# Optimization experiments

Measured on AMD Instinct MI355X. Metric: run time of the kernel, lower is better.

## Reference

```python
import jax, jax.numpy as jnp
import numpy as np

H = 256       # lstm_hidden_size
B = 64        # batch
L = 128       # sequence length
LABEL = 128   # slot label size


def setup_inputs() -> dict:
    key = jax.random.key(0)
    ks = jax.random.split(key, 8)
    s = 1.0 / np.sqrt(H)  # torch LSTM/Linear uniform init scale
    return {
        "x": jax.random.normal(ks[0], (B, L, 2 * H), jnp.float32),
        "hi": jax.random.normal(ks[1], (B, L, 2 * H), jnp.float32),
        "W_ih": jax.random.uniform(ks[2], (4 * H, 5 * H), jnp.float32, -s, s),
        "W_hh": jax.random.uniform(ks[3], (4 * H, H), jnp.float32, -s, s),
        "b_ih": jax.random.uniform(ks[4], (4 * H,), jnp.float32, -s, s),
        "b_hh": jax.random.uniform(ks[5], (4 * H,), jnp.float32, -s, s),
        "W_fc": jax.random.uniform(ks[6], (LABEL, H), jnp.float32, -s, s),
        "b_fc": jax.random.uniform(ks[7], (LABEL,), jnp.float32, -s, s),
    }


def reference(x, hi, W_ih, W_hh, b_ih, b_hh, W_fc, b_fc):
    # dropout_rate = 0.0 -> dropout is identity.
    h_dim = W_hh.shape[1]
    bias = b_ih + b_hh  # (4H,)

    # x cat hi: (B, L, 4H) -> time-major (L, B, 4H)
    feats = jnp.transpose(jnp.concatenate([x, hi], axis=-1), (1, 0, 2))

    def cell(hc, inp):
        # PyTorch feeds (batch,1,5H) into a seq-major LSTM, so each batch
        # element is one recurrent step with batch-size 1.
        h, c = hc  # (H,), (H,)
        g = inp @ W_ih.T + h @ W_hh.T + bias  # (4H,)
        i, f, gg, o = jnp.split(g, 4)
        i = jax.nn.sigmoid(i)
        f = jax.nn.sigmoid(f)
        gg = jnp.tanh(gg)
        o = jax.nn.sigmoid(o)
        c_new = f * c + i * gg
        h_new = o * jnp.tanh(c_new)
        return (h_new, c_new), h_new

    def step(carry, x_t):
        # x_t: (B, 4H); out_prev: (B, H) = previous timestep's LSTM outputs
        h, c, out_prev = carry
        inp = jnp.concatenate([x_t, out_prev], axis=-1)  # (B, 5H)
        (h, c), outs = jax.lax.scan(cell, (h, c), inp)   # scan over batch dim
        return (h, c, outs), outs

    h0 = jnp.zeros((h_dim,), x.dtype)
    c0 = jnp.zeros((h_dim,), x.dtype)
    out0 = jnp.zeros((x.shape[0], h_dim), x.dtype)  # dec_init_out

    (_, _, _), all_out = jax.lax.scan(step, (h0, c0, out0), feats)  # (L, B, H)
    output = jnp.transpose(all_out, (1, 0, 2))  # (B, L, H)
    return output @ W_fc.T + b_fc  # (B, L, LABEL)
```

## Files before the change

### kernel.cpp

```cpp
#include <hip/hip_runtime.h>
#include <math.h>

#define H    256
#define BB   64
#define LL   128
#define LBL  128
#define NSTEP (BB*LL)
#define GDIM (4*H)
#define KDIM (4*H)
#define W5   (5*H)
#define NWG  16
#define NROW (NSTEP + 64)

typedef unsigned long long ull;

#define SW(j) ((j) + ((j) >> 4))

__global__ void k_init(ull* __restrict__ HT)
{
    const int r = blockIdx.x;
    const int e = threadIdx.x;
    HT[(ull)r * H + e] = ((ull)(unsigned)r << 32);
}

__global__ __launch_bounds__(256) void k_pre(const float* __restrict__ x,
                                             const float* __restrict__ hi,
                                             const float* __restrict__ Wih,
                                             const float* __restrict__ bih,
                                             const float* __restrict__ bhh,
                                             _Float16* __restrict__ PREh)
{
    const int nb = blockIdx.x;
    const int t  = blockIdx.y;
    const int tid = threadIdx.x;
    const int tm = tid >> 4, tn = tid & 15;

    __shared__ float As[16][68];
    __shared__ float Bs[16][68];

    const int lm  = tid >> 2;
    const int lk4 = (tid & 3) * 4;

    float acc[4][4];
#pragma unroll
    for (int i = 0; i < 4; i++)
#pragma unroll
        for (int j = 0; j < 4; j++) acc[i][j] = 0.f;

    for (int j0 = 0; j0 < KDIM; j0 += 16) {
        const int j = j0 + lk4;
        float4 av;
        if (j < 512) av = *(const float4*)(x  + ((size_t)lm * LL + t) * 512 + j);
        else         av = *(const float4*)(hi + ((size_t)lm * LL + t) * 512 + (j - 512));
        float4 bv = *(const float4*)(Wih + (size_t)(nb * 64 + lm) * W5 + j);

        __syncthreads();
        As[lk4 + 0][lm] = av.x; As[lk4 + 1][lm] = av.y;
        As[lk4 + 2][lm] = av.z; As[lk4 + 3][lm] = av.w;
        Bs[lk4 + 0][lm] = bv.x; Bs[lk4 + 1][lm] = bv.y;
        Bs[lk4 + 2][lm] = bv.z; Bs[lk4 + 3][lm] = bv.w;
        __syncthreads();

#pragma unroll
        for (int kk = 0; kk < 16; kk++) {
            float4 a = *(const float4*)&As[kk][tm << 2];
            float4 b = *(const float4*)&Bs[kk][tn << 2];
            acc[0][0] += a.x * b.x; acc[0][1] += a.x * b.y; acc[0][2] += a.x * b.z; acc[0][3] += a.x * b.w;
            acc[1][0] += a.y * b.x; acc[1][1] += a.y * b.y; acc[1][2] += a.y * b.z; acc[1][3] += a.y * b.w;
            acc[2][0] += a.z * b.x; acc[2][1] += a.z * b.y; acc[2][2] += a.z * b.z; acc[2][3] += a.z * b.w;
            acc[3][0] += a.w * b.x; acc[3][1] += a.w * b.y; acc[3][2] += a.w * b.z; acc[3][3] += a.w * b.w;
        }
    }

    const int n0 = nb * 64 + tn * 4;
    float4 b1 = *(const float4*)(bih + n0);
    float4 b2 = *(const float4*)(bhh + n0);
    const float bx = b1.x + b2.x, by = b1.y + b2.y, bz = b1.z + b2.z, bw = b1.w + b2.w;
#pragma unroll
    for (int i = 0; i < 4; i++) {
        const size_t m = (size_t)t * 64 + tm * 4 + i;
        union { _Float16 h[4]; ull u; } p;
        p.h[0] = (_Float16)(acc[i][0] + bx);
        p.h[1] = (_Float16)(acc[i][1] + by);
        p.h[2] = (_Float16)(acc[i][2] + bz);
        p.h[3] = (_Float16)(acc[i][3] + bw);
        *(ull*)(PREh + m * GDIM + n0) = p.u;
    }
}

__device__ __forceinline__ float poll_pair(const ull* p, int want, long long& budget)
{
    ull v = __hip_atomic_load(p, __ATOMIC_RELAXED, __HIP_MEMORY_SCOPE_AGENT);
    while ((int)(v >> 32) != want) {
        if (--budget < 0) break;
        v = __hip_atomic_load(p, __ATOMIC_RELAXED, __HIP_MEMORY_SCOPE_AGENT);
    }
    union { unsigned u; float f; } c; c.u = (unsigned)v;
    return c.f;
}

__global__ __launch_bounds__(1024) void k_rec(const _Float16* __restrict__ PREh,
                                              const float* __restrict__ Wih,
                                              const float* __restrict__ Whh,
                                              ull* __restrict__ HT)
{
    const int g    = blockIdx.x;
    const int tid  = threadIdx.x;
    const int w    = tid >> 6;
    const int lane = tid & 63;
    const int gate = lane >> 4;
    const int kc   = lane & 15;
    const int j_own = g * 16 + w;
    const int row   = gate * H + j_own;

    float whh[16], wo[16];
#pragma unroll
    for (int i = 0; i < 16; i++) whh[i] = Whh[(size_t)row * H + kc * 16 + i];
#pragma unroll
    for (int i = 0; i < 16; i++) wo[i]  = Wih[(size_t)row * W5 + 4 * H + kc * 16 + i];

    __shared__ float h1s[2][272];
    __shared__ float h64s[2][272];

    long long budget = 8000000LL;

    if (lane < 32) {
        const int e  = (w << 4) + (kc);
        const int rw = (lane < 16) ? 63 : 0;
        float v = poll_pair(&HT[(ull)rw * H + e], rw, budget);
        if (lane < 16) h1s[0][SW(e)] = v; else h64s[0][SW(e)] = v;
    }
    float pre_cur = (float)PREh[row];
    float c_state = 0.f;
    __syncthreads();

    for (int k = 0; k < NSTEP; ++k) {
        const int cb = k & 1, nb = cb ^ 1;

        float acc = 0.f;
        const int base = kc * 17;
#pragma unroll
        for (int q = 0; q < 4; ++q) {
            float4 a = *(const float4*)&h1s[cb][base + 4 * q];
            acc += whh[4*q+0]*a.x + whh[4*q+1]*a.y + whh[4*q+2]*a.z + whh[4*q+3]*a.w;
        }
#pragma unroll
        for (int q = 0; q < 4; ++q) {
            float4 b = *(const float4*)&h64s[cb][base + 4 * q];
            acc += wo[4*q+0]*b.x + wo[4*q+1]*b.y + wo[4*q+2]*b.z + wo[4*q+3]*b.w;
        }
        acc += __shfl_xor(acc, 1);
        acc += __shfl_xor(acc, 2);
        acc += __shfl_xor(acc, 4);
        acc += __shfl_xor(acc, 8);
        acc += pre_cur;

        float act = (gate == 2) ? tanhf(acc) : 1.f / (1.f + __expf(-acc));
        const float iv = __shfl(act,      kc);
        const float fv = __shfl(act, 16 + kc);
        const float gv = __shfl(act, 32 + kc);
        const float ov = __shfl(act, 48 + kc);
        c_state = fv * c_state + iv * gv;
        const float h = ov * tanhf(c_state);

        if (lane == 0) {
            union { float f; unsigned u; } cv; cv.f = h;
            __hip_atomic_store(&HT[(ull)(k + 64) * H + j_own],
                               ((ull)(unsigned)(k + 64) << 32) | cv.u,
                               __ATOMIC_RELAXED, __HIP_MEMORY_SCOPE_AGENT);
            h1s[nb][SW(j_own)] = h;
        }

        float pre_next = 0.f;
        if (k + 1 < NSTEP) pre_next = (float)PREh[(size_t)(k + 1) * GDIM + row];

        if (lane < 32) {
            const int e = (w << 4) + kc;
            const bool own = (lane < 16) && (w == g);
            if (!own) {
                const int rw = (lane < 16) ? (k + 64) : (k + 1);
                float v = poll_pair(&HT[(ull)rw * H + e], rw, budget);
                if (lane < 16) h1s[nb][SW(e)] = v; else h64s[nb][SW(e)] = v;
            }
        }
        pre_cur = pre_next;
        __syncthreads();
    }
}

__global__ __launch_bounds__(256) void k_fc(const ull* __restrict__ HT,
                                            const float* __restrict__ Wfc,
                                            const float* __restrict__ bfc,
                                            float* __restrict__ out)
{
    __shared__ float hl[8 * 256];
    __shared__ float wl[128 * 65];
    const int blk = blockIdx.x;
    const int tid = threadIdx.x;

#pragma unroll
    for (int kk = 0; kk < 8; kk++) {
        ull v = HT[((ull)(blk * 8 + kk + 64)) * H + tid];
        union { unsigned u; float f; } c; c.u = (unsigned)v;
        hl[kk * 256 + tid] = c.f;
    }

    const int l = tid & 127, grp = tid >> 7;
    float a0 = 0.f, a1 = 0.f, a2 = 0.f, a3 = 0.f;

    for (int c = 0; c < 4; c++) {
        __syncthreads();
        for (int m = 0; m < 32; m++) {
            const int idx = m * 256 + tid;
            const int lr = idx >> 6, jc = idx & 63;
            wl[lr * 65 + jc] = Wfc[(size_t)lr * H + c * 64 + jc];
        }
        __syncthreads();
#pragma unroll 4
        for (int jc = 0; jc < 64; jc++) {
            const float wv = wl[l * 65 + jc];
            const int hj = c * 64 + jc;
            a0 += hl[(grp * 4 + 0) * 256 + hj] * wv;
            a1 += hl[(grp * 4 + 1) * 256 + hj] * wv;
            a2 += hl[(grp * 4 + 2) * 256 + hj] * wv;
            a3 += hl[(grp * 4 + 3) * 256 + hj] * wv;
        }
    }

    const float bias = bfc[l];
    float accs[4] = {a0, a1, a2, a3};
#pragma unroll
    for (int r = 0; r < 4; r++) {
        const int k = blk * 8 + grp * 4 + r;
        const int t = k >> 6, b = k & 63;
        out[((size_t)b * LL + t) * LBL + l] = accs[r] + bias;
    }
}

extern "C" void kernel_launch(void* const* d_in, const int* in_sizes, int n_in,
                              void* d_out, int out_size, void* d_ws, size_t ws_size,
                              hipStream_t stream)
{
    const float* x   = (const float*)d_in[0];
    const float* hi  = (const float*)d_in[1];
    const float* Wih = (const float*)d_in[2];
    const float* Whh = (const float*)d_in[3];
    const float* bih = (const float*)d_in[4];
    const float* bhh = (const float*)d_in[5];
    const float* Wfc = (const float*)d_in[6];
    const float* bfc = (const float*)d_in[7];
    float* out = (float*)d_out;

    _Float16* PREh = (_Float16*)d_ws;
    ull*      HT   = (ull*)((char*)d_ws +
                            (size_t)NSTEP * GDIM * sizeof(_Float16));

    const size_t need = (size_t)NSTEP * GDIM * sizeof(_Float16)
                      + (size_t)NROW * H * sizeof(ull);
    if (ws_size < need) return;

    k_init<<<64, H, 0, stream>>>(HT);
    k_pre<<<dim3(GDIM / 64, LL), 256, 0, stream>>>(x, hi, Wih, bih, bhh, PREh);
    k_rec<<<NWG, 1024, 0, stream>>>(PREh, Wih, Whh, HT);
    k_fc<<<NSTEP / 8, 256, 0, stream>>>(HT, Wfc, bfc, out);
}
```

Before: 18.49 ms.

## Run recurrence in a single workgroup with helper blocks computing lagged input projection

Measured after the change: 57.84 ms. 3.13x slower.

```diff
diff --git a/kernel.cpp b/kernel.cpp
--- a/kernel.cpp
+++ b/kernel.cpp
@@ -9,18 +9,60 @@
 #define GDIM (4*H)
 #define KDIM (4*H)
 #define W5   (5*H)
-#define NWG  16
 #define NROW (NSTEP + 64)
+#define NHELP 64
+#define ZRING 64
 
 typedef unsigned long long ull;
-
-#define SW(j) ((j) + ((j) >> 4))
-
-__global__ void k_init(ull* __restrict__ HT)
-{
-    const int r = blockIdx.x;
-    const int e = threadIdx.x;
-    HT[(ull)r * H + e] = ((ull)(unsigned)r << 32);
+typedef unsigned int u32;
+typedef _Float16 h2v __attribute__((ext_vector_type(2)));
+
+#if defined(__has_builtin)
+#  if __has_builtin(__builtin_amdgcn_fdot2)
+#    define HAVE_FDOT2 1
+#  endif
+#endif
+
+__device__ __forceinline__ float dot2f(u32 a, u32 b, float c)
+{
+    union { u32 u; h2v h; } ua, ub; ua.u = a; ub.u = b;
+#ifdef HAVE_FDOT2
+    return __builtin_amdgcn_fdot2(ua.h, ub.h, c, false);
+#else
+    return c + (float)ua.h[0]*(float)ub.h[0] + (float)ua.h[1]*(float)ub.h[1];
+#endif
+}
+
+__device__ __forceinline__ float tanh_fast(float x)
+{
+    const float ax = fabsf(x);
+    const float t  = __expf(-2.f*ax);
+    const float r  = (1.f - t)/(1.f + t);
+    return x >= 0.f ? r : -r;
+}
+
+__device__ __forceinline__ float sigm_fast(float x)
+{
+    return 1.f/(1.f + __expf(-x));
+}
+
+
+__global__ __launch_bounds__(256) void k_init(ull* __restrict__ HT,
+                                              ull* __restrict__ RUN)
+{
+    __shared__ u32 s_salt;
+    const int tid = threadIdx.x;
+    if (tid == 0) {
+        ull r = __hip_atomic_load(RUN, __ATOMIC_RELAXED, __HIP_MEMORY_SCOPE_AGENT) + 1;
+        __hip_atomic_store(RUN, r, __ATOMIC_RELAXED, __HIP_MEMORY_SCOPE_AGENT);
+        s_salt = (u32)r * 65536u;
+    }
+    __syncthreads();
+    const u32 salt = s_salt;
+    for (int i = tid; i < 64 * H; i += 256) {
+        const u32 r = (u32)(i >> 8);
+        HT[i] = ((ull)(salt + r) << 32);
+    }
 }
 
 __global__ __launch_bounds__(256) void k_pre(const float* __restrict__ x,
@@ -88,10 +130,9 @@
     }
 }
 
-__device__ __forceinline__ float poll_pair(const ull* p, int want, long long& budget)
-{
-    ull v = __hip_atomic_load(p, __ATOMIC_RELAXED, __HIP_MEMORY_SCOPE_AGENT);
-    while ((int)(v >> 32) != want) {
+__device__ __forceinline__ float z_wait(ull v, const ull* p, u32 want, long long& budget)
+{
+    while ((u32)(v >> 32) != want) {
         if (--budget < 0) break;
         v = __hip_atomic_load(p, __ATOMIC_RELAXED, __HIP_MEMORY_SCOPE_AGENT);
     }
@@ -99,92 +140,168 @@
     return c.f;
 }
 
-__global__ __launch_bounds__(1024) void k_rec(const _Float16* __restrict__ PREh,
-                                              const float* __restrict__ Wih,
-                                              const float* __restrict__ Whh,
-                                              ull* __restrict__ HT)
-{
-    const int g    = blockIdx.x;
-    const int tid  = threadIdx.x;
-    const int w    = tid >> 6;
-    const int lane = tid & 63;
-    const int gate = lane >> 4;
-    const int kc   = lane & 15;
-    const int j_own = g * 16 + w;
-    const int row   = gate * H + j_own;
-
-    float whh[16], wo[16];
-#pragma unroll
-    for (int i = 0; i < 16; i++) whh[i] = Whh[(size_t)row * H + kc * 16 + i];
-#pragma unroll
-    for (int i = 0; i < 16; i++) wo[i]  = Wih[(size_t)row * W5 + 4 * H + kc * 16 + i];
-
-    __shared__ float h1s[2][272];
-    __shared__ float h64s[2][272];
-
-    long long budget = 8000000LL;
-
-    if (lane < 32) {
-        const int e  = (w << 4) + (kc);
-        const int rw = (lane < 16) ? 63 : 0;
-        float v = poll_pair(&HT[(ull)rw * H + e], rw, budget);
-        if (lane < 16) h1s[0][SW(e)] = v; else h64s[0][SW(e)] = v;
-    }
-    float pre_cur = (float)PREh[row];
-    float c_state = 0.f;
-    __syncthreads();
-
-    for (int k = 0; k < NSTEP; ++k) {
-        const int cb = k & 1, nb = cb ^ 1;
-
-        float acc = 0.f;
-        const int base = kc * 17;
-#pragma unroll
-        for (int q = 0; q < 4; ++q) {
-            float4 a = *(const float4*)&h1s[cb][base + 4 * q];
-            acc += whh[4*q+0]*a.x + whh[4*q+1]*a.y + whh[4*q+2]*a.z + whh[4*q+3]*a.w;
-        }
-#pragma unroll
-        for (int q = 0; q < 4; ++q) {
-            float4 b = *(const float4*)&h64s[cb][base + 4 * q];
-            acc += wo[4*q+0]*b.x + wo[4*q+1]*b.y + wo[4*q+2]*b.z + wo[4*q+3]*b.w;
-        }
-        acc += __shfl_xor(acc, 1);
-        acc += __shfl_xor(acc, 2);
-        acc += __shfl_xor(acc, 4);
-        acc += __shfl_xor(acc, 8);
-        acc += pre_cur;
-
-        float act = (gate == 2) ? tanhf(acc) : 1.f / (1.f + __expf(-acc));
-        const float iv = __shfl(act,      kc);
-        const float fv = __shfl(act, 16 + kc);
-        const float gv = __shfl(act, 32 + kc);
-        const float ov = __shfl(act, 48 + kc);
-        c_state = fv * c_state + iv * gv;
-        const float h = ov * tanhf(c_state);
-
-        if (lane == 0) {
-            union { float f; unsigned u; } cv; cv.f = h;
-            __hip_atomic_store(&HT[(ull)(k + 64) * H + j_own],
-                               ((ull)(unsigned)(k + 64) << 32) | cv.u,
+__device__ __forceinline__ float poll_sleep(const ull* p, u32 want, long long& budget)
+{
+    ull v = __hip_atomic_load(p, __ATOMIC_RELAXED, __HIP_MEMORY_SCOPE_AGENT);
+    while ((u32)(v >> 32) != want) {
+        if (--budget < 0) break;
+        __builtin_amdgcn_s_sleep(16);
+        v = __hip_atomic_load(p, __ATOMIC_RELAXED, __HIP_MEMORY_SCOPE_AGENT);
+    }
+    union { unsigned u; float f; } c; c.u = (unsigned)v;
+    return c.f;
+}
+
+__global__ __launch_bounds__(512) void k_rec(const _Float16* __restrict__ PREh,
+                                             const float* __restrict__ Wih,
+                                             const float* __restrict__ Whh,
+                                             ull* __restrict__ HT,
+                                             ull* __restrict__ Z,
+                                             const ull* __restrict__ RUN)
+{
+    __shared__ uint4 wlds[8192];
+    __shared__ __align__(16) _Float16 hs[2][256];
+    __shared__ __align__(16) float hb[256];
+
+    const int tid = threadIdx.x;
+    const u32 salt = (u32)__hip_atomic_load(RUN, __ATOMIC_RELAXED,
+                                            __HIP_MEMORY_SCOPE_AGENT) * 65536u;
+
+    if (blockIdx.x == 0) {
+        const int e = tid >> 1;
+        const int h = tid & 1;
+
+        u32 wr[4][48];
+#pragma unroll
+        for (int g = 0; g < 4; ++g) {
+            const float* W = Whh + (size_t)(g*256 + e)*H + h*128;
+#pragma unroll
+            for (int c = 0; c < 48; ++c) {
+                float2 f = *(const float2*)(W + 2*c);
+                union { h2v hh; u32 u; } p;
+                p.hh[0] = (_Float16)f.x; p.hh[1] = (_Float16)f.y;
+                wr[g][c] = p.u;
+            }
+        }
+#pragma unroll
+        for (int g = 0; g < 4; ++g) {
+            const float* W = Whh + (size_t)(g*256 + e)*H + h*128 + 96;
+#pragma unroll
+            for (int d4 = 0; d4 < 4; ++d4) {
+                u32 u0, u1, u2, u3;
+                {
+                    float2 f; union { h2v hh; u32 uu; } p;
+                    f = *(const float2*)(W + 8*d4 + 0); p.hh[0]=(_Float16)f.x; p.hh[1]=(_Float16)f.y; u0 = p.uu;
+                    f = *(const float2*)(W + 8*d4 + 2); p.hh[0]=(_Float16)f.x; p.hh[1]=(_Float16)f.y; u1 = p.uu;
+                    f = *(const float2*)(W + 8*d4 + 4); p.hh[0]=(_Float16)f.x; p.hh[1]=(_Float16)f.y; u2 = p.uu;
+                    f = *(const float2*)(W + 8*d4 + 6); p.hh[0]=(_Float16)f.x; p.hh[1]=(_Float16)f.y; u3 = p.uu;
+                }
+                wlds[(d4*2 + h)*1024 + g*256 + e] = make_uint4(u0, u1, u2, u3);
+            }
+        }
+        if (tid < 128) ((u32*)hs[0])[tid] = 0u;
+
+        const ull* zp0 = Z + (size_t)(2*h    )*256 + e;
+        const ull* zp1 = Z + (size_t)(2*h + 1)*256 + e;
+        ull zc0 = __hip_atomic_load(zp0, __ATOMIC_RELAXED, __HIP_MEMORY_SCOPE_AGENT);
+        ull zc1 = __hip_atomic_load(zp1, __ATOMIC_RELAXED, __HIP_MEMORY_SCOPE_AGENT);
+
+        float c_state = 0.f;
+        long long budget = 2000000LL;
+        __syncthreads();
+
+        for (int k = 0; k < NSTEP; ++k) {
+            const size_t sl_n = (size_t)((k+1) & (ZRING-1)) * GDIM;
+            ull zn0 = __hip_atomic_load(zp0 + sl_n, __ATOMIC_RELAXED, __HIP_MEMORY_SCOPE_AGENT);
+            ull zn1 = __hip_atomic_load(zp1 + sl_n, __ATOMIC_RELAXED, __HIP_MEMORY_SCOPE_AGENT);
+
+            const uint4* hp = (const uint4*)((const char*)hs[k & 1] + h*256);
+            float acc[4] = {0.f, 0.f, 0.f, 0.f};
+#pragma unroll
+            for (int q = 0; q < 12; ++q) {
+                uint4 hv = hp[q];
+#pragma unroll
+                for (int g = 0; g < 4; ++g) {
+                    acc[g] = dot2f(wr[g][4*q+0], hv.x, acc[g]);
+                    acc[g] = dot2f(wr[g][4*q+1], hv.y, acc[g]);
+                    acc[g] = dot2f(wr[g][4*q+2], hv.z, acc[g]);
+                    acc[g] = dot2f(wr[g][4*q+3], hv.w, acc[g]);
+                }
+            }
+#pragma unroll
+            for (int q = 12; q < 16; ++q) {
+                uint4 hv = hp[q];
+                const int pl = (q - 12)*2 + h;
+#pragma unroll
+                for (int g = 0; g < 4; ++g) {
+                    uint4 wv = wlds[pl*1024 + g*256 + e];
+                    acc[g] = dot2f(wv.x, hv.x, acc[g]);
+                    acc[g] = dot2f(wv.y, hv.y, acc[g]);
+                    acc[g] = dot2f(wv.z, hv.z, acc[g]);
+                    acc[g] = dot2f(wv.w, hv.w, acc[g]);
+                }
+            }
+
+            const size_t sl = (size_t)(k & (ZRING-1)) * GDIM;
+            const u32 want = salt + (u32)k;
+            const float z0 = z_wait(zc0, zp0 + sl, want, budget);
+            const float z1 = z_wait(zc1, zp1 + sl, want, budget);
+            if (h == 0) { acc[0] += z0; acc[1] += z1; }
+            else        { acc[2] += z0; acc[3] += z1; }
+
+            const float s0 = acc[0] + __shfl_xor(acc[0], 1);
+            const float s1 = acc[1] + __shfl_xor(acc[1], 1);
+            const float s2 = acc[2] + __shfl_xor(acc[2], 1);
+            const float s3 = acc[3] + __shfl_xor(acc[3], 1);
+
+            const float iv = sigm_fast(s0);
+            const float fv = sigm_fast(s1);
+            const float gv = tanh_fast(s2);
+            const float ov = sigm_fast(s3);
+            c_state = fv * c_state + iv * gv;
+            const float hn = ov * tanh_fast(c_state);
+
+            if (h == 0) {
+                hs[(k + 1) & 1][e] = (_Float16)hn;
+                union { float f; unsigned u; } cv; cv.f = hn;
+                __hip_atomic_store(&HT[(ull)(k + 64) * H + e],
+                                   ((ull)(salt + (u32)(k + 64)) << 32) | cv.u,
+                                   __ATOMIC_RELAXED, __HIP_MEMORY_SCOPE_AGENT);
+            }
+            zc0 = zn0; zc1 = zn1;
+            __syncthreads();
+        }
+    } else {
+        const int wg = blockIdx.x - 1;
+        long long budget = 200000LL;
+        const int r0 = tid, r1 = tid + 512;
+        const float* w0 = Wih + (size_t)r0 * W5 + 4*H;
+        const float* w1 = Wih + (size_t)r1 * W5 + 4*H;
+
+        for (int k = wg; k < NSTEP; k += NHELP) {
+            if (tid < H) {
+                hb[tid] = poll_sleep(&HT[(ull)k * H + tid], salt + (u32)k, budget);
+            }
+            __syncthreads();
+
+            float a0 = (float)PREh[(size_t)k * GDIM + r0];
+            float a1 = (float)PREh[(size_t)k * GDIM + r1];
+#pragma unroll 4
+            for (int j = 0; j < H; j += 4) {
+                float4 hv = *(const float4*)(hb + j);
+                float4 wa = *(const float4*)(w0 + j);
+                float4 wb = *(const float4*)(w1 + j);
+                a0 += wa.x*hv.x + wa.y*hv.y + wa.z*hv.z + wa.w*hv.w;
+                a1 += wb.x*hv.x + wb.y*hv.y + wb.z*hv.z + wb.w*hv.w;
+            }
+            union { float f; unsigned u; } c0, c1; c0.f = a0; c1.f = a1;
+            const ull tg = (ull)(salt + (u32)k) << 32;
+            __hip_atomic_store(&Z[(size_t)(k & (ZRING-1))*GDIM + r0], tg | c0.u,
                                __ATOMIC_RELAXED, __HIP_MEMORY_SCOPE_AGENT);
-            h1s[nb][SW(j_own)] = h;
-        }
-
-        float pre_next = 0.f;
-        if (k + 1 < NSTEP) pre_next = (float)PREh[(size_t)(k + 1) * GDIM + row];
-
-        if (lane < 32) {
-            const int e = (w << 4) + kc;
-            const bool own = (lane < 16) && (w == g);
-            if (!own) {
-                const int rw = (lane < 16) ? (k + 64) : (k + 1);
-                float v = poll_pair(&HT[(ull)rw * H + e], rw, budget);
-                if (lane < 16) h1s[nb][SW(e)] = v; else h64s[nb][SW(e)] = v;
-            }
-        }
-        pre_cur = pre_next;
-        __syncthreads();
+            __hip_atomic_store(&Z[(size_t)(k & (ZRING-1))*GDIM + r1], tg | c1.u,
+                               __ATOMIC_RELAXED, __HIP_MEMORY_SCOPE_AGENT);
+            __syncthreads();
+        }
     }
 }
 
@@ -251,16 +368,20 @@
     const float* bfc = (const float*)d_in[7];
     float* out = (float*)d_out;
 
+    const size_t preh_b = (size_t)NSTEP * GDIM * sizeof(_Float16);
+    const size_t ht_b   = (size_t)NROW * H * sizeof(ull);
+    const size_t z_b    = (size_t)ZRING * GDIM * sizeof(ull);
+
     _Float16* PREh = (_Float16*)d_ws;
-    ull*      HT   = (ull*)((char*)d_ws +
-                            (size_t)NSTEP * GDIM * sizeof(_Float16));
-
-    const size_t need = (size_t)NSTEP * GDIM * sizeof(_Float16)
-                      + (size_t)NROW * H * sizeof(ull);
+    ull*      HT   = (ull*)((char*)d_ws + preh_b);
+    ull*      Zr   = (ull*)((char*)d_ws + preh_b + ht_b);
+    ull*      RUN  = (ull*)((char*)d_ws + preh_b + ht_b + z_b);
+
+    const size_t need = preh_b + ht_b + z_b + sizeof(ull);
     if (ws_size < need) return;
 
-    k_init<<<64, H, 0, stream>>>(HT);
+    k_init<<<1, 256, 0, stream>>>(HT, RUN);
     k_pre<<<dim3(GDIM / 64, LL), 256, 0, stream>>>(x, hi, Wih, bih, bhh, PREh);
-    k_rec<<<NWG, 1024, 0, stream>>>(PREh, Wih, Whh, HT);
+    k_rec<<<1 + NHELP, 512, 0, stream>>>(PREh, Wih, Whh, HT, Zr, RUN);
     k_fc<<<NSTEP / 8, 256, 0, stream>>>(HT, Wfc, bfc, out);
 }
```
